# Optimization experiments

Measured on AMD Instinct MI355X. Metric: run time of the kernel, lower is better.

Reference implementation:

```python
import jax, jax.numpy as jnp
import numpy as np

E = 1024  # hidden_size
H = 16    # num_heads
D = E // H  # head_dim
LN_EPS = 1e-5


def setup_inputs() -> dict:
    key = jax.random.key(0)
    ks = jax.random.split(key, 7)
    B, S = 4, 2048
    scale = 1.0 / np.sqrt(E)
    return {
        "txt_emb": jax.random.normal(ks[0], (B, S, E), dtype=jnp.float32),
        "in_proj_w": jax.random.normal(ks[1], (3 * E, E), dtype=jnp.float32) * scale,
        "in_proj_b": jnp.zeros((3 * E,), dtype=jnp.float32),
        "out_proj_w": jax.random.normal(ks[2], (E, E), dtype=jnp.float32) * scale,
        "out_proj_b": jnp.zeros((E,), dtype=jnp.float32),
        "ln_gamma": jnp.ones((E,), dtype=jnp.float32),
        "ln_beta": jnp.zeros((E,), dtype=jnp.float32),
    }


def _layer_norm(x, gamma, beta):
    mu = jnp.mean(x, axis=-1, keepdims=True)
    var = jnp.var(x, axis=-1, keepdims=True)
    return (x - mu) * jax.lax.rsqrt(var + LN_EPS) * gamma + beta


def reference(txt_emb, in_proj_w, in_proj_b, out_proj_w, out_proj_b, ln_gamma, ln_beta):
    B, S, _ = txt_emb.shape
    # joint QKV projection (torch nn.MultiheadAttention semantics: x @ W.T + b)
    qkv = jnp.einsum('bse,fe->bsf', txt_emb, in_proj_w) + in_proj_b  # [B,S,3E]
    q, k, v = jnp.split(qkv, 3, axis=-1)
    # [B,H,S,D]
    q = q.reshape(B, S, H, D).transpose(0, 2, 1, 3)
    k = k.reshape(B, S, H, D).transpose(0, 2, 1, 3)
    v = v.reshape(B, S, H, D).transpose(0, 2, 1, 3)
    scores = jnp.einsum('bhqd,bhkd->bhqk', q, k) / np.sqrt(D)  # [B,H,S,S]
    causal = jnp.tril(jnp.ones((S, S), dtype=bool))
    scores = jnp.where(causal, scores, jnp.float32(-jnp.inf))
    attn = jax.nn.softmax(scores, axis=-1)
    ctx = jnp.einsum('bhqk,bhkd->bhqd', attn, v)  # [B,H,S,D]
    ctx = ctx.transpose(0, 2, 1, 3).reshape(B, S, E)
    attn_out = jnp.einsum('bse,fe->bsf', ctx, out_proj_w) + out_proj_b
    return _layer_norm(txt_emb + attn_out, ln_gamma, ln_beta)
```

## Files before the change

### kernel.cpp

```cpp
#include <hip/hip_runtime.h>
#include <hip/hip_bf16.h>
#include <stdint.h>

#define B_   4
#define S_   2048
#define E_   1024
#define H_   16
#define D_   64
#define M_   (B_ * S_)
#define E3_  (3 * E_)

#define QSCALE 0.18033688011112042f

typedef __bf16 bf16_t;
typedef bf16_t bf16x8 __attribute__((ext_vector_type(8)));
typedef float  f32x4  __attribute__((ext_vector_type(4)));
typedef float  f32x16 __attribute__((ext_vector_type(16)));

__device__ __forceinline__ ushort f2bf(float f) {
  union { float f; uint32_t u; } v; v.f = f;
  uint32_t r = v.u + 0x7fffu + ((v.u >> 16) & 1u);
  return (ushort)(r >> 16);
}

__device__ __forceinline__ unsigned cvtpk(float lo, float hi_) {
  unsigned d;
  asm("v_cvt_pk_bf16_f32 %0, %1, %2" : "=v"(d) : "v"(lo), "v"(hi_));
  return d;
}

__device__ __forceinline__ void gload_lds16(const void* g, void* l) {
  __builtin_amdgcn_global_load_lds((const __attribute__((address_space(1))) void*)g,
                                   (__attribute__((address_space(3))) void*)l,
                                   16, 0, 0);
}

__global__ __launch_bounds__(256) void cvt_f32_bf16(const float* __restrict__ in,
                                                    ushort* __restrict__ out, int n4,
                                                    int scale_row4, float scale) {
  int i = blockIdx.x * blockDim.x + threadIdx.x;
  if (i < n4) {
    float4 v = reinterpret_cast<const float4*>(in)[i];
    if (i < scale_row4) { v.x *= scale; v.y *= scale; v.z *= scale; v.w *= scale; }
    ushort4 o;
    o.x = f2bf(v.x); o.y = f2bf(v.y); o.z = f2bf(v.z); o.w = f2bf(v.w);
    reinterpret_cast<ushort4*>(out)[i] = o;
  }
}

template <int MODE>
__global__ __launch_bounds__(256) void gemm_bt(const ushort* __restrict__ A,
                                               const ushort* __restrict__ Bt,
                                               const float* __restrict__ bias,
                                               void* __restrict__ out0,
                                               ushort* __restrict__ vTout,
                                               int Mdim, int Ndim, int K) {
  __shared__ __align__(16) ushort As[128 * 32];
  __shared__ __align__(16) ushort Bs[128 * 32];

  const int tid  = threadIdx.x;
  const int lane = tid & 63, wid = tid >> 6;
  const int wr = wid >> 1, wc = wid & 1;

  const int nx = gridDim.x;
  const int nwg = nx * gridDim.y;
  const int b0 = blockIdx.y * nx + blockIdx.x;
  const int nb = (b0 & 7) * (nwg >> 3) + (b0 >> 3);
  const int bm = (nb / nx) * 128, bn = (nb % nx) * 128;

  const int lrow = lane & 15, lk8 = (lane >> 4) * 8, lg4 = (lane >> 4) * 4;
  const int srow = tid >> 2;
  const int skk  = (tid & 3) * 8;

  f32x4 acc[4][4] = {};

  for (int k0 = 0; k0 < K; k0 += 32) {
#pragma unroll
    for (int j = 0; j < 2; ++j) {
      const ushort* ga = A  + (size_t)(bm + j * 64 + srow) * K + k0 + skk;
      const ushort* gb = Bt + (size_t)(bn + j * 64 + srow) * K + k0 + skk;
      gload_lds16(ga, (void*)&As[(j * 256 + wid * 64) * 8]);
      gload_lds16(gb, (void*)&Bs[(j * 256 + wid * 64) * 8]);
    }
    __syncthreads();

    bf16x8 af[4], bfv[4];
#pragma unroll
    for (int rb = 0; rb < 4; ++rb)
      af[rb] = *reinterpret_cast<const bf16x8*>(&As[(wr * 64 + rb * 16 + lrow) * 32 + lk8]);
#pragma unroll
    for (int cb = 0; cb < 4; ++cb)
      bfv[cb] = *reinterpret_cast<const bf16x8*>(&Bs[(wc * 64 + cb * 16 + lrow) * 32 + lk8]);
#pragma unroll
    for (int rb = 0; rb < 4; ++rb)
#pragma unroll
      for (int cb = 0; cb < 4; ++cb)
        acc[rb][cb] = __builtin_amdgcn_mfma_f32_16x16x32_bf16(af[rb], bfv[cb], acc[rb][cb], 0, 0, 0);
    __syncthreads();
  }

#pragma unroll
  for (int rb = 0; rb < 4; ++rb) {
#pragma unroll
    for (int cb = 0; cb < 4; ++cb) {
      const int col = bn + wc * 64 + cb * 16 + lrow;
      float bv = bias[col];
      if (MODE == 1 && col < 1024) bv *= QSCALE;
      const int row0 = bm + wr * 64 + rb * 16 + lg4;
      if (MODE == 0) {
#pragma unroll
        for (int r = 0; r < 4; ++r)
          ((float*)out0)[(size_t)(row0 + r) * Ndim + col] = acc[rb][cb][r] + bv;
      } else {
        if (col < 2048) {
#pragma unroll
          for (int r = 0; r < 4; ++r)
            ((ushort*)out0)[(size_t)(row0 + r) * 2048 + col] = f2bf(acc[rb][cb][r] + bv);
        } else {
          ushort4 vv;
          vv.x = f2bf(acc[rb][cb][0] + bv);
          vv.y = f2bf(acc[rb][cb][1] + bv);
          vv.z = f2bf(acc[rb][cb][2] + bv);
          vv.w = f2bf(acc[rb][cb][3] + bv);
          const size_t vidx = ((size_t)((row0 >> 11) * 1024 + (col - 2048))) * 2048 + (row0 & 2047);
          *reinterpret_cast<ushort4*>(&vTout[vidx]) = vv;
        }
      }
    }
  }
}

__global__ __launch_bounds__(512) void attn_causal(const ushort* __restrict__ qk,
                                                   const ushort* __restrict__ vT,
                                                   ushort* __restrict__ ctx) {
  __shared__ __align__(16) char lds[2][16384];

  const int tid = threadIdx.x;
  const int w = tid >> 6, lane = tid & 63;
  const int l31 = lane & 31, hi = lane >> 5;

  const int bid = blockIdx.x;
  const int bh = (bid & 7) * 8 + ((bid >> 3) & 7);
  const int g6 = bid >> 6;
  const int qb = (g6 < 4) ? (7 - g6) : (g6 - 4);
  const int b = bh >> 4, h = bh & 15;
  const int qbase = qb * 256;
  const int tmax = 4 * qb + 3;
  const int qw = qbase + w * 32;
  const int q_g = qw + l31;
  const int my_tmax = (qw + 31) >> 6;

  const ushort* qrow = qk + (size_t)(b * S_ + q_g) * 2048 + h * 64;
  bf16x8 qf[4];
#pragma unroll
  for (int st = 0; st < 4; ++st)
    qf[st] = *reinterpret_cast<const bf16x8*>(qrow + st * 16 + hi * 8);

  const int srow = tid >> 3;
  const int swz  = ((tid & 7) * 16) ^ ((srow & 7) << 4);
  const char* kbase = (const char*)qk + ((size_t)(b * S_ + srow) * 2048 + 1024 + h * 64) * 2 + swz;
  const char* vbase = (const char*)vT + ((size_t)(bh * 64 + srow) * 2048) * 2 + swz;

  f32x16 Ot0 = {}, Ot1 = {};
  float m_r = -__builtin_inff(), l_r = 0.f;

  const int kswz = ((l31 & 7) << 4);

#define STAGE(T, BUFI)                                                              \
  do {                                                                              \
    gload_lds16(kbase + (size_t)(T) * (64 * 2048 * 2), &lds[BUFI][w * 1024]);       \
    gload_lds16(vbase + (size_t)(T) * 128,             &lds[BUFI][8192 + w * 1024]);\
  } while (0)

  STAGE(0, 0);
  for (int t = 0; t <= tmax; ++t) {
    const int bufi = t & 1;
    if (t < tmax) {
      STAGE(t + 1, bufi ^ 1);
      asm volatile("s_waitcnt vmcnt(2)" ::: "memory");
    } else {
      asm volatile("s_waitcnt vmcnt(0)" ::: "memory");
    }
    __builtin_amdgcn_s_barrier();
    __builtin_amdgcn_sched_barrier(0);

    if (t <= my_tmax) {
      const char* Kt = &lds[bufi][0];
      const char* Vp = &lds[bufi][8192];

      f32x16 T0 = {}, T1 = {};
#pragma unroll
      for (int st = 0; st < 4; ++st) {
        const int cb = (st * 32 + hi * 16) ^ kswz;
        bf16x8 k0 = *(const bf16x8*)(Kt + l31 * 128 + cb);
        bf16x8 k1 = *(const bf16x8*)(Kt + (32 + l31) * 128 + cb);
        T0 = __builtin_amdgcn_mfma_f32_32x32x16_bf16(k0, qf[st], T0, 0, 0, 0);
        T1 = __builtin_amdgcn_mfma_f32_32x32x16_bf16(k1, qf[st], T1, 0, 0, 0);
      }

      float p[32];
      const bool needmask = (t * 64 + 63) > qw;
      const int kvb = t * 64 + 4 * hi;
#pragma unroll
      for (int g = 0; g < 4; ++g) {
#pragma unroll
        for (int j = 0; j < 4; ++j) {
          float v0 = T0[4 * g + j], v1 = T1[4 * g + j];
          if (needmask) {
            const int kv0 = kvb + 8 * g + j;
            v0 = (kv0      <= q_g) ? v0 : -__builtin_inff();
            v1 = (kv0 + 32 <= q_g) ? v1 : -__builtin_inff();
          }
          p[4 * g + j] = v0;
          p[16 + 4 * g + j] = v1;
        }
      }
      float pmax = p[0];
#pragma unroll
      for (int i = 1; i < 31; i += 2) pmax = fmaxf(fmaxf(pmax, p[i]), p[i + 1]);
      pmax = fmaxf(pmax, p[31]);
      pmax = fmaxf(pmax, __shfl_xor(pmax, 32));

      if (!__all(pmax - m_r <= 8.f)) {
        const float mn = fmaxf(m_r, pmax);
        const float sc = exp2f(m_r - mn);
        m_r = mn;
        l_r *= sc;
#pragma unroll
        for (int i = 0; i < 16; ++i) { Ot0[i] *= sc; Ot1[i] *= sc; }
      }
      float sum = 0.f;
#pragma unroll
      for (int i = 0; i < 32; ++i) { p[i] = exp2f(p[i] - m_r); sum += p[i]; }
      sum += __shfl_xor(sum, 32);
      l_r += sum;

#pragma unroll
      for (int ks = 0; ks < 4; ++ks) {
        const unsigned a = cvtpk(p[8 * ks + 0], p[8 * ks + 1]);
        const unsigned bq = cvtpk(p[8 * ks + 2], p[8 * ks + 3]);
        const unsigned c = cvtpk(p[8 * ks + 4], p[8 * ks + 5]);
        const unsigned d = cvtpk(p[8 * ks + 6], p[8 * ks + 7]);
        const unsigned x = hi ? a : c;
        const unsigned y = hi ? bq : d;
        const unsigned xp = (unsigned)__shfl_xor((int)x, 32);
        const unsigned yp = (unsigned)__shfl_xor((int)y, 32);
        union { unsigned u[4]; bf16x8 v; } pa;
        pa.u[0] = hi ? xp : a;
        pa.u[1] = hi ? yp : bq;
        pa.u[2] = hi ? c : xp;
        pa.u[3] = hi ? d : yp;
        const int cb = (ks * 32 + hi * 16) ^ kswz;
        bf16x8 v0 = *(const bf16x8*)(Vp + l31 * 128 + cb);
        bf16x8 v1 = *(const bf16x8*)(Vp + (32 + l31) * 128 + cb);
        Ot0 = __builtin_amdgcn_mfma_f32_32x32x16_bf16(v0, pa.v, Ot0, 0, 0, 0);
        Ot1 = __builtin_amdgcn_mfma_f32_32x32x16_bf16(v1, pa.v, Ot1, 0, 0, 0);
      }
    }
    __builtin_amdgcn_s_barrier();
    __builtin_amdgcn_sched_barrier(0);
  }

  const float inv = 1.0f / l_r;
  ushort* crow = ctx + (size_t)(b * S_ + q_g) * 1024 + h * 64;
#pragma unroll
  for (int g = 0; g < 4; ++g) {
#pragma unroll
    for (int jp = 0; jp < 2; ++jp) {
      const int d0 = 2 * jp + 8 * g + 4 * hi;
      const int r = 4 * g + 2 * jp;
      *(unsigned*)(crow + d0)      = cvtpk(Ot0[r] * inv, Ot0[r + 1] * inv);
      *(unsigned*)(crow + 32 + d0) = cvtpk(Ot1[r] * inv, Ot1[r + 1] * inv);
    }
  }
#undef STAGE
}

__global__ __launch_bounds__(256) void resid_ln(const float* __restrict__ x,
                                                const float* __restrict__ ao,
                                                const float* __restrict__ gamma,
                                                const float* __restrict__ beta,
                                                float* __restrict__ out) {
  const int row = blockIdx.x;
  const int tid = threadIdx.x;
  const size_t base = (size_t)row * E_;

  float4 xv = reinterpret_cast<const float4*>(x + base)[tid];
  float4 av = reinterpret_cast<const float4*>(ao + base)[tid];
  const float v0 = xv.x + av.x, v1 = xv.y + av.y, v2 = xv.z + av.z, v3 = xv.w + av.w;
  float s  = v0 + v1 + v2 + v3;
  float s2 = v0 * v0 + v1 * v1 + v2 * v2 + v3 * v3;
#pragma unroll
  for (int off = 32; off >= 1; off >>= 1) {
    s  += __shfl_xor(s, off);
    s2 += __shfl_xor(s2, off);
  }
  __shared__ float red[8];
  const int wid = tid >> 6, lane = tid & 63;
  if (lane == 0) { red[wid] = s; red[4 + wid] = s2; }
  __syncthreads();
  s  = red[0] + red[1] + red[2] + red[3];
  s2 = red[4] + red[5] + red[6] + red[7];
  const float mu  = s * (1.f / E_);
  const float var = s2 * (1.f / E_) - mu * mu;
  const float rsd = rsqrtf(var + 1e-5f);

  float4 gv = reinterpret_cast<const float4*>(gamma)[tid];
  float4 bv = reinterpret_cast<const float4*>(beta)[tid];
  float4 ov;
  ov.x = (v0 - mu) * rsd * gv.x + bv.x;
  ov.y = (v1 - mu) * rsd * gv.y + bv.y;
  ov.z = (v2 - mu) * rsd * gv.z + bv.z;
  ov.w = (v3 - mu) * rsd * gv.w + bv.w;
  reinterpret_cast<float4*>(out + base)[tid] = ov;
}

extern "C" void kernel_launch(void* const* d_in, const int* in_sizes, int n_in,
                              void* d_out, int out_size, void* d_ws, size_t ws_size,
                              hipStream_t stream) {
  (void)in_sizes; (void)n_in; (void)out_size; (void)ws_size;
  const float* x     = (const float*)d_in[0];
  const float* w_in  = (const float*)d_in[1];
  const float* b_in  = (const float*)d_in[2];
  const float* w_out = (const float*)d_in[3];
  const float* b_out = (const float*)d_in[4];
  const float* gamma = (const float*)d_in[5];
  const float* beta  = (const float*)d_in[6];
  float* out = (float*)d_out;

  char* ws = (char*)d_ws;
  ushort* xb    = (ushort*)(ws);
  ushort* winb  = (ushort*)(ws + 16777216);
  ushort* woutb = (ushort*)(ws + 23068672);
  ushort* qkb   = (ushort*)(ws + 25165824);
  ushort* vTb   = (ushort*)(ws + 58720256);
  ushort* ctxb  = (ushort*)(ws + 75497472);
  float*  ao    = (float*)(ws + 92274688);

  cvt_f32_bf16<<<dim3((M_ * E_) / 4 / 256), 256, 0, stream>>>(x, xb, (M_ * E_) / 4, 0, 1.f);
  cvt_f32_bf16<<<dim3((E3_ * E_) / 4 / 256), 256, 0, stream>>>(w_in, winb, (E3_ * E_) / 4,
                                                               (E_ * E_) / 4, QSCALE);
  cvt_f32_bf16<<<dim3((E_ * E_) / 4 / 256), 256, 0, stream>>>(w_out, woutb, (E_ * E_) / 4, 0, 1.f);

  gemm_bt<1><<<dim3(E3_ / 128, M_ / 128), 256, 0, stream>>>(xb, winb, b_in, qkb, vTb, M_, E3_, E_);
  attn_causal<<<dim3(512), 512, 0, stream>>>(qkb, vTb, ctxb);
  gemm_bt<0><<<dim3(E_ / 128, M_ / 128), 256, 0, stream>>>(ctxb, woutb, b_out, ao, nullptr, M_, E_, E_);
  resid_ln<<<dim3(M_), 256, 0, stream>>>(x, ao, gamma, beta, out);
}
```

Baseline: 213.1 us.

## Replace QKV GEMM with 256x256-tile double-buffered 8-wave kernel

Adds a dedicated QKV projection kernel that uses 256x256 output tiles with K=64 steps, 512 threads and double-buffered LDS filled by direct global-to-LDS loads. It uses XOR-swizzled LDS addressing and splits the MFMA work into phases under explicit barriers and priority hints. The aim is more data reuse per tile and overlap of the next tile's loads with compute. The cost is heavy LDS use (128KB) and high register pressure, which limit occupancy to one block per CU, and the grid shrinks to 384 blocks.

After: 221.3 us. 3.8% more time.

```diff
diff --git a/kernel.cpp b/kernel.cpp
--- a/kernel.cpp
+++ b/kernel.cpp
@@ -48,13 +48,152 @@
   }
 }
 
-template <int MODE>
-__global__ __launch_bounds__(256) void gemm_bt(const ushort* __restrict__ A,
-                                               const ushort* __restrict__ Bt,
-                                               const float* __restrict__ bias,
-                                               void* __restrict__ out0,
-                                               ushort* __restrict__ vTout,
-                                               int Mdim, int Ndim, int K) {
+__global__ __launch_bounds__(512) void gemm_qkv_256(const ushort* __restrict__ A,
+                                                    const ushort* __restrict__ Bt,
+                                                    const float* __restrict__ bias,
+                                                    ushort* __restrict__ qkout,
+                                                    ushort* __restrict__ vTout) {
+  __shared__ __align__(16) ushort As[2][256 * 64];
+  __shared__ __align__(16) ushort Bs[2][256 * 64];
+
+  const int tid = threadIdx.x;
+  const int lane = tid & 63, wid = tid >> 6;
+  const int wr = wid >> 2, wc = wid & 3;
+
+  const int b0 = blockIdx.x;
+  const int nb = (b0 & 7) * 48 + (b0 >> 3);
+  const int bm = (nb / 12) * 256, bn = (nb % 12) * 256;
+
+  const int l8 = lane >> 3;
+  const int scol8 = (lane & 7) ^ l8;
+  const ushort* aSrc = A  + (size_t)(bm + wr * 128 + wc * 32 + l8) * 1024 + scol8 * 8;
+  const ushort* bSrc = Bt + (size_t)(bn + wc * 64 + wr * 32 + l8) * 1024 + scol8 * 8;
+
+#define STAGE8(T, BI)                                                                        \
+  do {                                                                                       \
+    _Pragma("unroll")                                                                        \
+    for (int j = 0; j < 4; ++j)                                                              \
+      gload_lds16(aSrc + (T) * 64 + j * 8192, (void*)&As[BI][(wr * 128 + wc * 32 + j * 8) * 64]); \
+    _Pragma("unroll")                                                                        \
+    for (int j = 0; j < 4; ++j)                                                              \
+      gload_lds16(bSrc + (T) * 64 + j * 8192, (void*)&Bs[BI][(wc * 64 + wr * 32 + j * 8) * 64]); \
+  } while (0)
+
+  const int arow = wr * 128 + (lane & 15);
+  const int brow = wc * 64 + (lane & 15);
+  const int sl0 = (((lane >> 4) + 0) ^ (lane & 7)) * 16;
+  const int sl1 = (((lane >> 4) + 4) ^ (lane & 7)) * 16;
+
+#define LDA(dst, m, p)                                                                     \
+  do {                                                                                     \
+    dst[0] = *(const bf16x8*)((const char*)&As[p][0] + (arow + (m) * 16) * 128 + sl0);     \
+    dst[1] = *(const bf16x8*)((const char*)&As[p][0] + (arow + (m) * 16) * 128 + sl1);     \
+  } while (0)
+#define LDB(dst, n, p)                                                                     \
+  do {                                                                                     \
+    dst[0] = *(const bf16x8*)((const char*)&Bs[p][0] + (brow + (n) * 16) * 128 + sl0);     \
+    dst[1] = *(const bf16x8*)((const char*)&Bs[p][0] + (brow + (n) * 16) * 128 + sl1);     \
+  } while (0)
+
+#define BARRIER_FENCE()                        \
+  do {                                         \
+    __builtin_amdgcn_s_barrier();              \
+    __builtin_amdgcn_sched_barrier(0);         \
+  } while (0)
+
+#define MFMA16(MB, NB)                                                                      \
+  do {                                                                                      \
+    __builtin_amdgcn_s_setprio(1);                                                          \
+    _Pragma("unroll")                                                                       \
+    for (int m = 0; m < 4; ++m)                                                             \
+      _Pragma("unroll")                                                                     \
+      for (int n = 0; n < 2; ++n)                                                           \
+        _Pragma("unroll")                                                                   \
+        for (int kh = 0; kh < 2; ++kh)                                                      \
+          acc[(MB) + m][(NB) + n] = __builtin_amdgcn_mfma_f32_16x16x32_bf16(                \
+              af[m][kh], bf[n][kh], acc[(MB) + m][(NB) + n], 0, 0, 0);                      \
+    __builtin_amdgcn_s_setprio(0);                                                          \
+  } while (0)
+
+  f32x4 acc[8][4] = {};
+  bf16x8 af[4][2], bf[2][2];
+
+  STAGE8(0, 0);
+  asm volatile("s_waitcnt vmcnt(0)" ::: "memory");
+  BARRIER_FENCE();
+
+  for (int t = 0; t < 16; ++t) {
+    const int p = t & 1;
+    if (t < 15) STAGE8(t + 1, p ^ 1);
+#pragma unroll
+    for (int m = 0; m < 4; ++m) LDA(af[m], m, p);
+#pragma unroll
+    for (int n = 0; n < 2; ++n) LDB(bf[n], n, p);
+    __builtin_amdgcn_s_barrier();
+    asm volatile("s_waitcnt lgkmcnt(0)" ::: "memory");
+    __builtin_amdgcn_sched_barrier(0);
+    MFMA16(0, 0);
+    BARRIER_FENCE();
+#pragma unroll
+    for (int n = 0; n < 2; ++n) LDB(bf[n], n + 2, p);
+    __builtin_amdgcn_s_barrier();
+    asm volatile("s_waitcnt lgkmcnt(0)" ::: "memory");
+    __builtin_amdgcn_sched_barrier(0);
+    MFMA16(0, 2);
+    BARRIER_FENCE();
+#pragma unroll
+    for (int m = 0; m < 4; ++m) LDA(af[m], m + 4, p);
+    __builtin_amdgcn_s_barrier();
+    asm volatile("s_waitcnt lgkmcnt(0)" ::: "memory");
+    __builtin_amdgcn_sched_barrier(0);
+    MFMA16(4, 2);
+    BARRIER_FENCE();
+#pragma unroll
+    for (int n = 0; n < 2; ++n) LDB(bf[n], n, p);
+    __builtin_amdgcn_s_barrier();
+    asm volatile("s_waitcnt lgkmcnt(0)" ::: "memory");
+    __builtin_amdgcn_sched_barrier(0);
+    MFMA16(4, 0);
+    if (t < 15) asm volatile("s_waitcnt vmcnt(0)" ::: "memory");
+    BARRIER_FENCE();
+  }
+
+  const int lr = lane & 15, lg4 = (lane >> 4) * 4;
+#pragma unroll
+  for (int m = 0; m < 8; ++m) {
+#pragma unroll
+    for (int n = 0; n < 4; ++n) {
+      const int col = bn + wc * 64 + n * 16 + lr;
+      float bv = bias[col];
+      if (col < 1024) bv *= QSCALE;
+      const int row0 = bm + wr * 128 + m * 16 + lg4;
+      if (col < 2048) {
+#pragma unroll
+        for (int r = 0; r < 4; ++r)
+          qkout[(size_t)(row0 + r) * 2048 + col] = f2bf(acc[m][n][r] + bv);
+      } else {
+        ushort4 vv;
+        vv.x = f2bf(acc[m][n][0] + bv);
+        vv.y = f2bf(acc[m][n][1] + bv);
+        vv.z = f2bf(acc[m][n][2] + bv);
+        vv.w = f2bf(acc[m][n][3] + bv);
+        const size_t vidx = ((size_t)((row0 >> 11) * 1024 + (col - 2048))) * 2048 + (row0 & 2047);
+        *reinterpret_cast<ushort4*>(&vTout[vidx]) = vv;
+      }
+    }
+  }
+#undef STAGE8
+#undef LDA
+#undef LDB
+#undef BARRIER_FENCE
+#undef MFMA16
+}
+
+__global__ __launch_bounds__(256) void gemm_bt0(const ushort* __restrict__ A,
+                                                const ushort* __restrict__ Bt,
+                                                const float* __restrict__ bias,
+                                                float* __restrict__ out0,
+                                                int Mdim, int Ndim, int K) {
   __shared__ __align__(16) ushort As[128 * 32];
   __shared__ __align__(16) ushort Bs[128 * 32];
 
@@ -104,28 +243,11 @@
 #pragma unroll
     for (int cb = 0; cb < 4; ++cb) {
       const int col = bn + wc * 64 + cb * 16 + lrow;
-      float bv = bias[col];
-      if (MODE == 1 && col < 1024) bv *= QSCALE;
+      const float bv = bias[col];
       const int row0 = bm + wr * 64 + rb * 16 + lg4;
-      if (MODE == 0) {
-#pragma unroll
-        for (int r = 0; r < 4; ++r)
-          ((float*)out0)[(size_t)(row0 + r) * Ndim + col] = acc[rb][cb][r] + bv;
-      } else {
-        if (col < 2048) {
-#pragma unroll
-          for (int r = 0; r < 4; ++r)
-            ((ushort*)out0)[(size_t)(row0 + r) * 2048 + col] = f2bf(acc[rb][cb][r] + bv);
-        } else {
-          ushort4 vv;
-          vv.x = f2bf(acc[rb][cb][0] + bv);
-          vv.y = f2bf(acc[rb][cb][1] + bv);
-          vv.z = f2bf(acc[rb][cb][2] + bv);
-          vv.w = f2bf(acc[rb][cb][3] + bv);
-          const size_t vidx = ((size_t)((row0 >> 11) * 1024 + (col - 2048))) * 2048 + (row0 & 2047);
-          *reinterpret_cast<ushort4*>(&vTout[vidx]) = vv;
-        }
-      }
+#pragma unroll
+      for (int r = 0; r < 4; ++r)
+        out0[(size_t)(row0 + r) * Ndim + col] = acc[rb][cb][r] + bv;
     }
   }
 }
@@ -342,8 +464,8 @@
                                                                (E_ * E_) / 4, QSCALE);
   cvt_f32_bf16<<<dim3((E_ * E_) / 4 / 256), 256, 0, stream>>>(w_out, woutb, (E_ * E_) / 4, 0, 1.f);
 
-  gemm_bt<1><<<dim3(E3_ / 128, M_ / 128), 256, 0, stream>>>(xb, winb, b_in, qkb, vTb, M_, E3_, E_);
+  gemm_qkv_256<<<dim3(384), 512, 0, stream>>>(xb, winb, b_in, qkb, vTb);
   attn_causal<<<dim3(512), 512, 0, stream>>>(qkb, vTb, ctxb);
-  gemm_bt<0><<<dim3(E_ / 128, M_ / 128), 256, 0, stream>>>(ctxb, woutb, b_out, ao, nullptr, M_, E_, E_);
+  gemm_bt0<<<dim3(E_ / 128, M_ / 128), 256, 0, stream>>>(ctxb, woutb, b_out, ao, M_, E_, E_);
   resid_ln<<<dim3(M_), 256, 0, stream>>>(x, ao, gamma, beta, out);
 }
```

## Replace QKV GEMM with triple-buffered 128x256 tile kernel using direct LDS loads

Applied to the files above, without the earlier changes.

The QKV projection moves to a new kernel with 512 threads and 128x256 output tiles over K-steps of 64. It triple-buffers LDS, filling it with global_load_lds. A swizzled LDS layout avoids bank conflicts, and explicit waitcnt, barriers and setprio interleave prefetch of tile t+2 with MFMA on tile t. The goal is to hide global-memory latency and raise MFMA utilisation over the old single-buffered 128x128 kernel. In exchange it uses 144KB of LDS, which limits occupancy to one block per CU, and it is hard-coded to these shapes.

After: 212.0 us. No clear change (-0.5%).

```diff
diff --git a/kernel.cpp b/kernel.cpp
--- a/kernel.cpp
+++ b/kernel.cpp
@@ -48,13 +48,142 @@
   }
 }
 
-template <int MODE>
-__global__ __launch_bounds__(256) void gemm_bt(const ushort* __restrict__ A,
-                                               const ushort* __restrict__ Bt,
-                                               const float* __restrict__ bias,
-                                               void* __restrict__ out0,
-                                               ushort* __restrict__ vTout,
-                                               int Mdim, int Ndim, int K) {
+__global__ __launch_bounds__(512) void gemm_qkv_8ph(const ushort* __restrict__ A,
+                                                    const ushort* __restrict__ Bt,
+                                                    const float* __restrict__ bias,
+                                                    ushort* __restrict__ qkout,
+                                                    ushort* __restrict__ vTout) {
+  __shared__ __align__(16) char lds[3][49152];
+
+  const int tid = threadIdx.x;
+  const int lane = tid & 63, wid = tid >> 6;
+  const int wr = wid >> 2, wc = wid & 3;
+
+  const int b0 = blockIdx.x;
+  const int nb = (b0 & 7) * 96 + (b0 >> 3);
+  const int bm = (nb / 12) * 128;
+  const int bn = (nb % 12) * 256;
+
+  const int l8 = lane >> 3;
+  const int sw = (lane & 7) ^ l8;
+  const ushort* aS = A  + (size_t)(bm + wid * 16 + l8) * 1024 + sw * 8;
+  const ushort* bS = Bt + (size_t)(bn + wid * 32 + l8) * 1024 + sw * 8;
+
+#define STAGE_A(T, BUF, J) \
+  gload_lds16(aS + (size_t)(T) * 64 + (J) * 8 * 1024, (void*)((BUF) + (wid * 2 + (J)) * 1024))
+#define STAGE_B(T, BUF, J) \
+  gload_lds16(bS + (size_t)(T) * 64 + (J) * 8 * 1024, (void*)((BUF) + 16384 + (wid * 4 + (J)) * 1024))
+
+  const int lr15 = lane & 15;
+  const int ksub = lane >> 4;
+  const int slot0 = ((ksub + 0) ^ (lr15 & 7)) * 16;
+  const int slot1 = ((ksub + 4) ^ (lr15 & 7)) * 16;
+  const int arow_b = (wr * 64 + lr15) * 128;
+  const int brow_b = (wc * 64 + lr15) * 128;
+
+#define LDA_ALL(BUF)                                                              \
+  do {                                                                            \
+    _Pragma("unroll")                                                             \
+    for (int m = 0; m < 4; ++m) {                                                 \
+      af[m][0] = *(const bf16x8*)((BUF) + arow_b + m * 2048 + slot0);             \
+      af[m][1] = *(const bf16x8*)((BUF) + arow_b + m * 2048 + slot1);             \
+    }                                                                             \
+  } while (0)
+#define LDB2(BUF, NB)                                                             \
+  do {                                                                            \
+    _Pragma("unroll")                                                             \
+    for (int n = 0; n < 2; ++n) {                                                 \
+      bfr[n][0] = *(const bf16x8*)((BUF) + 16384 + brow_b + ((NB) + n) * 2048 + slot0); \
+      bfr[n][1] = *(const bf16x8*)((BUF) + 16384 + brow_b + ((NB) + n) * 2048 + slot1); \
+    }                                                                             \
+  } while (0)
+#define MFMA16(NB)                                                                \
+  do {                                                                            \
+    __builtin_amdgcn_s_setprio(1);                                                \
+    _Pragma("unroll")                                                             \
+    for (int m = 0; m < 4; ++m)                                                   \
+      _Pragma("unroll")                                                           \
+      for (int n = 0; n < 2; ++n)                                                 \
+        _Pragma("unroll")                                                         \
+        for (int kh = 0; kh < 2; ++kh)                                            \
+          acc[m][(NB) + n] = __builtin_amdgcn_mfma_f32_16x16x32_bf16(             \
+              af[m][kh], bfr[n][kh], acc[m][(NB) + n], 0, 0, 0);                  \
+    __builtin_amdgcn_s_setprio(0);                                                \
+  } while (0)
+
+  f32x4 acc[4][4] = {};
+  bf16x8 af[4][2], bfr[2][2];
+
+  char* buf0 = &lds[0][0];
+  char* buf1 = &lds[1][0];
+  char* buf2 = &lds[2][0];
+
+  STAGE_A(0, buf0, 0); STAGE_A(0, buf0, 1);
+  STAGE_B(0, buf0, 0); STAGE_B(0, buf0, 1); STAGE_B(0, buf0, 2); STAGE_B(0, buf0, 3);
+  STAGE_A(1, buf1, 0); STAGE_A(1, buf1, 1);
+  STAGE_B(1, buf1, 0); STAGE_B(1, buf1, 1); STAGE_B(1, buf1, 2); STAGE_B(1, buf1, 3);
+  asm volatile("s_waitcnt vmcnt(6)" ::: "memory");
+  __builtin_amdgcn_s_barrier();
+  __builtin_amdgcn_sched_barrier(0);
+
+  for (int t = 0; t < 16; ++t) {
+    if (t < 14) { STAGE_A(t + 2, buf2, 0); STAGE_A(t + 2, buf2, 1); STAGE_B(t + 2, buf2, 0); }
+    LDA_ALL(buf0);
+    LDB2(buf0, 0);
+    __builtin_amdgcn_s_barrier();
+    asm volatile("s_waitcnt lgkmcnt(0)" ::: "memory");
+    __builtin_amdgcn_sched_barrier(0);
+    MFMA16(0);
+    __builtin_amdgcn_s_barrier();
+    __builtin_amdgcn_sched_barrier(0);
+    if (t < 14) { STAGE_B(t + 2, buf2, 1); STAGE_B(t + 2, buf2, 2); STAGE_B(t + 2, buf2, 3); }
+    LDB2(buf0, 2);
+    __builtin_amdgcn_s_barrier();
+    asm volatile("s_waitcnt lgkmcnt(0)" ::: "memory");
+    __builtin_amdgcn_sched_barrier(0);
+    MFMA16(2);
+    if (t < 14) asm volatile("s_waitcnt vmcnt(6)" ::: "memory");
+    else if (t == 14) asm volatile("s_waitcnt vmcnt(0)" ::: "memory");
+    __builtin_amdgcn_s_barrier();
+    __builtin_amdgcn_sched_barrier(0);
+    char* tmp = buf0; buf0 = buf1; buf1 = buf2; buf2 = tmp;
+  }
+
+#pragma unroll
+  for (int m = 0; m < 4; ++m) {
+#pragma unroll
+    for (int n = 0; n < 4; ++n) {
+      const int col = bn + wc * 64 + n * 16 + lr15;
+      float bv = bias[col];
+      if (col < 1024) bv *= QSCALE;
+      const int row0 = bm + wr * 64 + m * 16 + ksub * 4;
+      if (col < 2048) {
+#pragma unroll
+        for (int r = 0; r < 4; ++r)
+          qkout[(size_t)(row0 + r) * 2048 + col] = f2bf(acc[m][n][r] + bv);
+      } else {
+        ushort4 vv;
+        vv.x = f2bf(acc[m][n][0] + bv);
+        vv.y = f2bf(acc[m][n][1] + bv);
+        vv.z = f2bf(acc[m][n][2] + bv);
+        vv.w = f2bf(acc[m][n][3] + bv);
+        const size_t vidx = ((size_t)((row0 >> 11) * 1024 + (col - 2048))) * 2048 + (row0 & 2047);
+        *reinterpret_cast<ushort4*>(&vTout[vidx]) = vv;
+      }
+    }
+  }
+#undef STAGE_A
+#undef STAGE_B
+#undef LDA_ALL
+#undef LDB2
+#undef MFMA16
+}
+
+__global__ __launch_bounds__(256) void gemm_bt0(const ushort* __restrict__ A,
+                                                const ushort* __restrict__ Bt,
+                                                const float* __restrict__ bias,
+                                                float* __restrict__ out0,
+                                                int Mdim, int Ndim, int K) {
   __shared__ __align__(16) ushort As[128 * 32];
   __shared__ __align__(16) ushort Bs[128 * 32];
 
@@ -104,28 +233,11 @@
 #pragma unroll
     for (int cb = 0; cb < 4; ++cb) {
       const int col = bn + wc * 64 + cb * 16 + lrow;
-      float bv = bias[col];
-      if (MODE == 1 && col < 1024) bv *= QSCALE;
+      const float bv = bias[col];
       const int row0 = bm + wr * 64 + rb * 16 + lg4;
-      if (MODE == 0) {
-#pragma unroll
-        for (int r = 0; r < 4; ++r)
-          ((float*)out0)[(size_t)(row0 + r) * Ndim + col] = acc[rb][cb][r] + bv;
-      } else {
-        if (col < 2048) {
-#pragma unroll
-          for (int r = 0; r < 4; ++r)
-            ((ushort*)out0)[(size_t)(row0 + r) * 2048 + col] = f2bf(acc[rb][cb][r] + bv);
-        } else {
-          ushort4 vv;
-          vv.x = f2bf(acc[rb][cb][0] + bv);
-          vv.y = f2bf(acc[rb][cb][1] + bv);
-          vv.z = f2bf(acc[rb][cb][2] + bv);
-          vv.w = f2bf(acc[rb][cb][3] + bv);
-          const size_t vidx = ((size_t)((row0 >> 11) * 1024 + (col - 2048))) * 2048 + (row0 & 2047);
-          *reinterpret_cast<ushort4*>(&vTout[vidx]) = vv;
-        }
-      }
+#pragma unroll
+      for (int r = 0; r < 4; ++r)
+        out0[(size_t)(row0 + r) * Ndim + col] = acc[rb][cb][r] + bv;
     }
   }
 }
@@ -342,8 +454,8 @@
                                                                (E_ * E_) / 4, QSCALE);
   cvt_f32_bf16<<<dim3((E_ * E_) / 4 / 256), 256, 0, stream>>>(w_out, woutb, (E_ * E_) / 4, 0, 1.f);
 
-  gemm_bt<1><<<dim3(E3_ / 128, M_ / 128), 256, 0, stream>>>(xb, winb, b_in, qkb, vTb, M_, E3_, E_);
+  gemm_qkv_8ph<<<dim3(768), 512, 0, stream>>>(xb, winb, b_in, qkb, vTb);
   attn_causal<<<dim3(512), 512, 0, stream>>>(qkb, vTb, ctxb);
-  gemm_bt<0><<<dim3(E_ / 128, M_ / 128), 256, 0, stream>>>(ctxb, woutb, b_out, ao, nullptr, M_, E_, E_);
+  gemm_bt0<<<dim3(E_ / 128, M_ / 128), 256, 0, stream>>>(ctxb, woutb, b_out, ao, M_, E_, E_);
   resid_ln<<<dim3(M_), 256, 0, stream>>>(x, ao, gamma, beta, out);
 }
```

## Triple-buffer GEMM LDS staging with swizzled layout and interleaved MFMA scheduling

Applied to the files above, without the earlier changes.

Replaces the single-buffered bf16 GEMM with a three-stage LDS ring. Global-to-LDS loads for tile t+2 are issued while tile t is being computed, with explicit vmcnt/lgkmcnt waits and barriers. It adds an XOR swizzle on the LDS k-slot to avoid bank conflicts, splits the MFMA work into halves under raised s_setprio, and moves to a 1D grid. The goal is to hide global load latency and remove the two full syncthreads per k-step, at the cost of 48KB of LDS per block, which may reduce occupancy.

Result: faster. 202.1 us (-5.2%).

```diff
diff --git a/kernel.cpp b/kernel.cpp
--- a/kernel.cpp
+++ b/kernel.cpp
@@ -49,64 +49,117 @@
 }
 
 template <int MODE>
-__global__ __launch_bounds__(256) void gemm_bt(const ushort* __restrict__ A,
-                                               const ushort* __restrict__ Bt,
-                                               const float* __restrict__ bias,
-                                               void* __restrict__ out0,
-                                               ushort* __restrict__ vTout,
-                                               int Mdim, int Ndim, int K) {
-  __shared__ __align__(16) ushort As[128 * 32];
-  __shared__ __align__(16) ushort Bs[128 * 32];
+__global__ __launch_bounds__(256) void gemm_bt2(const ushort* __restrict__ A,
+                                                const ushort* __restrict__ Bt,
+                                                const float* __restrict__ bias,
+                                                void* __restrict__ out0,
+                                                ushort* __restrict__ vTout,
+                                                int Ndim, int K) {
+  __shared__ __align__(16) char lds[3][16384];
 
   const int tid  = threadIdx.x;
   const int lane = tid & 63, wid = tid >> 6;
+  const int w = wid;
   const int wr = wid >> 1, wc = wid & 1;
 
-  const int nx = gridDim.x;
-  const int nwg = nx * gridDim.y;
-  const int b0 = blockIdx.y * nx + blockIdx.x;
-  const int nb = (b0 & 7) * (nwg >> 3) + (b0 >> 3);
-  const int bm = (nb / nx) * 128, bn = (nb % nx) * 128;
-
-  const int lrow = lane & 15, lk8 = (lane >> 4) * 8, lg4 = (lane >> 4) * 4;
-  const int srow = tid >> 2;
-  const int skk  = (tid & 3) * 8;
+  const int nx  = Ndim >> 7;
+  const int nwg = gridDim.x;
+  const int b0  = blockIdx.x;
+  const int nb  = (b0 & 7) * (nwg >> 3) + (b0 >> 3);
+  const int bm  = (nb / nx) * 128, bn = (nb % nx) * 128;
+
+  const int srow  = tid >> 2;
+  const int sslot = (tid & 3) ^ (srow & 3) ^ ((srow >> 2) & 3);
+  const ushort* aS = A  + (size_t)(bm + srow) * K + sslot * 8;
+  const ushort* bS = Bt + (size_t)(bn + srow) * K + sslot * 8;
+
+#define STAGE_A(T, BUF)                                                          \
+  do {                                                                           \
+    gload_lds16(aS + (size_t)(T) * 32,              (void*)((BUF) + w * 1024));  \
+    gload_lds16(aS + (size_t)(T) * 32 + 64 * K,     (void*)((BUF) + 4096 + w * 1024)); \
+  } while (0)
+#define STAGE_B(T, BUF)                                                          \
+  do {                                                                           \
+    gload_lds16(bS + (size_t)(T) * 32,              (void*)((BUF) + 8192 + w * 1024)); \
+    gload_lds16(bS + (size_t)(T) * 32 + 64 * K,     (void*)((BUF) + 12288 + w * 1024)); \
+  } while (0)
+
+  const int lr15 = lane & 15;
+  const int ksub = lane >> 4;
+  const int slot = (ksub ^ (lr15 & 3) ^ ((lr15 >> 2) & 3)) * 16;
+  const int arow_b = (wr * 64 + lr15) * 64;
+  const int brow_b = 8192 + (wc * 64 + lr15) * 64;
+
+#define LDA4(BUF)                                                                \
+  do {                                                                           \
+    _Pragma("unroll")                                                            \
+    for (int rb = 0; rb < 4; ++rb)                                               \
+      af[rb] = *(const bf16x8*)((BUF) + arow_b + rb * 1024 + slot);              \
+  } while (0)
+#define LDB2(BUF, CB)                                                            \
+  do {                                                                           \
+    _Pragma("unroll")                                                            \
+    for (int n = 0; n < 2; ++n)                                                  \
+      bfr[n] = *(const bf16x8*)((BUF) + brow_b + ((CB) + n) * 1024 + slot);      \
+  } while (0)
+#define MFMA8(CB)                                                                \
+  do {                                                                           \
+    __builtin_amdgcn_s_setprio(1);                                               \
+    _Pragma("unroll")                                                            \
+    for (int rb = 0; rb < 4; ++rb)                                               \
+      _Pragma("unroll")                                                          \
+      for (int n = 0; n < 2; ++n)                                                \
+        acc[rb][(CB) + n] = __builtin_amdgcn_mfma_f32_16x16x32_bf16(             \
+            af[rb], bfr[n], acc[rb][(CB) + n], 0, 0, 0);                         \
+    __builtin_amdgcn_s_setprio(0);                                               \
+  } while (0)
 
   f32x4 acc[4][4] = {};
-
-  for (int k0 = 0; k0 < K; k0 += 32) {
-#pragma unroll
-    for (int j = 0; j < 2; ++j) {
-      const ushort* ga = A  + (size_t)(bm + j * 64 + srow) * K + k0 + skk;
-      const ushort* gb = Bt + (size_t)(bn + j * 64 + srow) * K + k0 + skk;
-      gload_lds16(ga, (void*)&As[(j * 256 + wid * 64) * 8]);
-      gload_lds16(gb, (void*)&Bs[(j * 256 + wid * 64) * 8]);
-    }
-    __syncthreads();
-
-    bf16x8 af[4], bfv[4];
-#pragma unroll
-    for (int rb = 0; rb < 4; ++rb)
-      af[rb] = *reinterpret_cast<const bf16x8*>(&As[(wr * 64 + rb * 16 + lrow) * 32 + lk8]);
-#pragma unroll
-    for (int cb = 0; cb < 4; ++cb)
-      bfv[cb] = *reinterpret_cast<const bf16x8*>(&Bs[(wc * 64 + cb * 16 + lrow) * 32 + lk8]);
-#pragma unroll
-    for (int rb = 0; rb < 4; ++rb)
-#pragma unroll
-      for (int cb = 0; cb < 4; ++cb)
-        acc[rb][cb] = __builtin_amdgcn_mfma_f32_16x16x32_bf16(af[rb], bfv[cb], acc[rb][cb], 0, 0, 0);
-    __syncthreads();
+  bf16x8 af[4], bfr[2];
+
+  char* buf0 = &lds[0][0];
+  char* buf1 = &lds[1][0];
+  char* buf2 = &lds[2][0];
+
+  const int nt = K >> 5;
+
+  STAGE_A(0, buf0); STAGE_B(0, buf0);
+  STAGE_A(1, buf1); STAGE_B(1, buf1);
+  asm volatile("s_waitcnt vmcnt(4)" ::: "memory");
+  __builtin_amdgcn_s_barrier();
+  __builtin_amdgcn_sched_barrier(0);
+
+  for (int t = 0; t < nt; ++t) {
+    if (t < nt - 2) STAGE_A(t + 2, buf2);
+    LDA4(buf0);
+    LDB2(buf0, 0);
+    __builtin_amdgcn_s_barrier();
+    asm volatile("s_waitcnt lgkmcnt(0)" ::: "memory");
+    __builtin_amdgcn_sched_barrier(0);
+    MFMA8(0);
+    __builtin_amdgcn_s_barrier();
+    __builtin_amdgcn_sched_barrier(0);
+    if (t < nt - 2) STAGE_B(t + 2, buf2);
+    LDB2(buf0, 2);
+    __builtin_amdgcn_s_barrier();
+    asm volatile("s_waitcnt lgkmcnt(0)" ::: "memory");
+    __builtin_amdgcn_sched_barrier(0);
+    MFMA8(2);
+    if (t < nt - 2) asm volatile("s_waitcnt vmcnt(4)" ::: "memory");
+    else if (t == nt - 2) asm volatile("s_waitcnt vmcnt(0)" ::: "memory");
+    __builtin_amdgcn_s_barrier();
+    __builtin_amdgcn_sched_barrier(0);
+    char* tmp = buf0; buf0 = buf1; buf1 = buf2; buf2 = tmp;
   }
 
 #pragma unroll
   for (int rb = 0; rb < 4; ++rb) {
 #pragma unroll
     for (int cb = 0; cb < 4; ++cb) {
-      const int col = bn + wc * 64 + cb * 16 + lrow;
+      const int col = bn + wc * 64 + cb * 16 + lr15;
       float bv = bias[col];
       if (MODE == 1 && col < 1024) bv *= QSCALE;
-      const int row0 = bm + wr * 64 + rb * 16 + lg4;
+      const int row0 = bm + wr * 64 + rb * 16 + ksub * 4;
       if (MODE == 0) {
 #pragma unroll
         for (int r = 0; r < 4; ++r)
@@ -128,6 +181,11 @@
       }
     }
   }
+#undef STAGE_A
+#undef STAGE_B
+#undef LDA4
+#undef LDB2
+#undef MFMA8
 }
 
 __global__ __launch_bounds__(512) void attn_causal(const ushort* __restrict__ qk,
@@ -342,8 +400,8 @@
                                                                (E_ * E_) / 4, QSCALE);
   cvt_f32_bf16<<<dim3((E_ * E_) / 4 / 256), 256, 0, stream>>>(w_out, woutb, (E_ * E_) / 4, 0, 1.f);
 
-  gemm_bt<1><<<dim3(E3_ / 128, M_ / 128), 256, 0, stream>>>(xb, winb, b_in, qkb, vTb, M_, E3_, E_);
+  gemm_bt2<1><<<dim3(1536), 256, 0, stream>>>(xb, winb, b_in, qkb, vTb, E3_, E_);
   attn_causal<<<dim3(512), 512, 0, stream>>>(qkb, vTb, ctxb);
-  gemm_bt<0><<<dim3(E_ / 128, M_ / 128), 256, 0, stream>>>(ctxb, woutb, b_out, ao, nullptr, M_, E_, E_);
+  gemm_bt2<0><<<dim3(512), 256, 0, stream>>>(ctxb, woutb, b_out, ao, nullptr, E_, E_);
   resid_ln<<<dim3(M_), 256, 0, stream>>>(x, ao, gamma, beta, out);
 }
```
